# Kernel tuning notes

Hardware: AMD Instinct MI355X
Metric: run time of the kernel (lower is better)

Reference implementation:

```python
import jax, jax.numpy as jnp
import numpy as np

N = 128
INSTANCES = 64
EMBED_DIM = 256
HIDDEN = 1024
BATCH = 2048


def _kaiming(key, dims):
    # matches custom_kaiming: randn * sqrt(2 / dims[-2])
    return jax.random.normal(key, dims, dtype=jnp.float32) * np.sqrt(2.0 / float(dims[-2])).astype(np.float32)


def setup_inputs() -> dict:
    key = jax.random.key(0)
    k_a, k_el, k_er, k_lin, k_un = jax.random.split(key, 5)
    a = jax.random.randint(k_a, (BATCH, 2), 0, N, dtype=jnp.int64 if jax.config.jax_enable_x64 else jnp.int32)
    return {
        "a": a,
        "embedding_left": _kaiming(k_el, (INSTANCES, N, EMBED_DIM)),
        "embedding_right": _kaiming(k_er, (INSTANCES, N, EMBED_DIM)),
        "linear": _kaiming(k_lin, (INSTANCES, EMBED_DIM, HIDDEN)),
        "unembedding": _kaiming(k_un, (INSTANCES, HIDDEN, N)),
    }


def reference(a, embedding_left, embedding_right, linear, unembedding):
    # one-hot @ embedding == direct gather along the vocab axis (same math, O(1) per lookup)
    a1, a2 = a[:, 0], a[:, 1]
    # [instances, batch, embed] -> [batch, instances, embed]
    x1 = jnp.transpose(jnp.take(embedding_left, a1, axis=1), (1, 0, 2))
    x2 = jnp.transpose(jnp.take(embedding_right, a2, axis=1), (1, 0, 2))
    hidden = jnp.einsum('bie,ieh->bih', x1 + x2, linear)
    out = jnp.einsum('bih,ihn->bin', jax.nn.gelu(hidden, approximate=False), unembedding)
    return out
```

## Files before the change

### kernel.cpp

```cpp
#include <hip/hip_runtime.h>
#include <hip/hip_bf16.h>

typedef __bf16 bf16;
typedef __bf16 bf16x4 __attribute__((ext_vector_type(4)));
typedef __bf16 bf16x8 __attribute__((ext_vector_type(8)));
typedef float  f32x4  __attribute__((ext_vector_type(4)));

#define MFMA16(A,B,C) __builtin_amdgcn_mfma_f32_16x16x32_bf16((A),(B),(C),0,0,0)

constexpr int NI    = 64;
constexpr int NN    = 128;
constexpr int E     = 256;
constexpr int HID   = 1024;
constexpr int BATCH = 2048;
constexpr int BM    = 128;
constexpr int BH    = 64;
constexpr int W1P   = E  + 8;
constexpr int W2P   = BH + 8;
constexpr int HP    = BH + 8;

__device__ __forceinline__ float fast_gelu(float x) {
    float p = 1.5957691216f * __builtin_fmaf(0.044715f * x * x, x, x);
    return x * __builtin_amdgcn_rcpf(1.0f + __expf(-p));
}

__global__ __launch_bounds__(256, 2) void mlp3_fused(
    const int*   __restrict__ a,
    const float* __restrict__ embL,
    const float* __restrict__ embR,
    const float* __restrict__ W1,
    const float* __restrict__ W2,
    float* __restrict__ out)
{
    __shared__ __align__(16) bf16 sW1[BH][W1P];
    __shared__ __align__(16) bf16 sW2[NN][W2P];
    __shared__ __align__(16) bf16 sH [BM][HP];

    const int blk   = blockIdx.x;
    const int xcd   = blk & 7;
    const int j     = blk >> 3;
    const int inst  = xcd + 8 * (j >> 4);
    const int btile = j & 15;

    const int tid  = threadIdx.x;
    const int wave = tid >> 6;
    const int lane = tid & 63;
    const int m = lane & 15;
    const int q = lane >> 4;

    bf16x8 aF[2][8];
    #pragma unroll
    for (int rt = 0; rt < 2; ++rt) {
        const int r  = btile * BM + wave * 32 + rt * 16 + m;
        const int i1 = a[2 * r + 0];
        const int i2 = a[2 * r + 1];
        const float* pl = embL + ((size_t)inst * NN + i1) * E;
        const float* pr = embR + ((size_t)inst * NN + i2) * E;
        #pragma unroll
        for (int ks = 0; ks < 8; ++ks) {
            const int e0 = ks * 32 + q * 8;
            f32x4 l0 = *(const f32x4*)(pl + e0);
            f32x4 l1 = *(const f32x4*)(pl + e0 + 4);
            f32x4 r0 = *(const f32x4*)(pr + e0);
            f32x4 r1 = *(const f32x4*)(pr + e0 + 4);
            bf16x8 s;
            #pragma unroll
            for (int k = 0; k < 4; ++k) {
                s[k]     = (bf16)(l0[k] + r0[k]);
                s[k + 4] = (bf16)(l1[k] + r1[k]);
            }
            aF[rt][ks] = s;
        }
    }

    f32x4 O[2][8];
    #pragma unroll
    for (int rt = 0; rt < 2; ++rt)
        #pragma unroll
        for (int ct = 0; ct < 8; ++ct)
            O[rt][ct] = (f32x4){0.f, 0.f, 0.f, 0.f};

    const int w1_h0 = (tid & 15) * 4;
    const int w1_eq = (tid >> 4) * 4;
    const int w2_n0 = (tid & 31) * 4;
    const int w2_hq = (tid >> 5) * 4;

    #pragma unroll 1
    for (int c = 0; c < HID / BH; ++c) {
        __syncthreads();

        {
            const float* base = W1 + ((size_t)inst * E + w1_eq) * HID + c * BH + w1_h0;
            #pragma unroll
            for (int s = 0; s < 4; ++s) {
                f32x4 v[4];
                #pragma unroll
                for (int k = 0; k < 4; ++k)
                    v[k] = *(const f32x4*)(base + ((size_t)s * 64 + k) * HID);
                #pragma unroll
                for (int jj = 0; jj < 4; ++jj) {
                    bf16x4 w;
                    #pragma unroll
                    for (int k = 0; k < 4; ++k) w[k] = (bf16)v[k][jj];
                    *(bf16x4*)&sW1[w1_h0 + jj][s * 64 + w1_eq] = w;
                }
            }
        }
        {
            const float* base = W2 + ((size_t)inst * HID + c * BH + w2_hq) * NN + w2_n0;
            #pragma unroll
            for (int s = 0; s < 2; ++s) {
                f32x4 v[4];
                #pragma unroll
                for (int k = 0; k < 4; ++k)
                    v[k] = *(const f32x4*)(base + ((size_t)s * 32 + k) * NN);
                #pragma unroll
                for (int jj = 0; jj < 4; ++jj) {
                    bf16x4 w;
                    #pragma unroll
                    for (int k = 0; k < 4; ++k) w[k] = (bf16)v[k][jj];
                    *(bf16x4*)&sW2[w2_n0 + jj][s * 32 + w2_hq] = w;
                }
            }
        }
        __syncthreads();

        f32x4 S[2][4];
        #pragma unroll
        for (int rt = 0; rt < 2; ++rt)
            #pragma unroll
            for (int ct = 0; ct < 4; ++ct) S[rt][ct] = (f32x4){0.f, 0.f, 0.f, 0.f};
        #pragma unroll
        for (int ks = 0; ks < 8; ++ks) {
            #pragma unroll
            for (int ct = 0; ct < 4; ++ct) {
                bf16x8 b = *(const bf16x8*)&sW1[ct * 16 + m][ks * 32 + q * 8];
                S[0][ct] = MFMA16(aF[0][ks], b, S[0][ct]);
                S[1][ct] = MFMA16(aF[1][ks], b, S[1][ct]);
            }
        }

        #pragma unroll
        for (int rt = 0; rt < 2; ++rt)
            #pragma unroll
            for (int ct = 0; ct < 4; ++ct)
                #pragma unroll
                for (int rr = 0; rr < 4; ++rr)
                    sH[wave * 32 + rt * 16 + q * 4 + rr][ct * 16 + m] =
                        (bf16)fast_gelu(S[rt][ct][rr]);
        asm volatile("s_waitcnt lgkmcnt(0)" ::: "memory");

        #pragma unroll
        for (int k2 = 0; k2 < 2; ++k2) {
            bf16x8 h0 = *(const bf16x8*)&sH[wave * 32 +  0 + m][k2 * 32 + q * 8];
            bf16x8 h1 = *(const bf16x8*)&sH[wave * 32 + 16 + m][k2 * 32 + q * 8];
            #pragma unroll
            for (int ct = 0; ct < 8; ++ct) {
                bf16x8 b = *(const bf16x8*)&sW2[ct * 16 + m][k2 * 32 + q * 8];
                O[0][ct] = MFMA16(h0, b, O[0][ct]);
                O[1][ct] = MFMA16(h1, b, O[1][ct]);
            }
        }
    }

    #pragma unroll
    for (int rt = 0; rt < 2; ++rt)
        #pragma unroll
        for (int ct = 0; ct < 8; ++ct)
            #pragma unroll
            for (int rr = 0; rr < 4; ++rr) {
                const int b = btile * BM + wave * 32 + rt * 16 + q * 4 + rr;
                const int n = ct * 16 + m;
                out[((size_t)b * NI + inst) * NN + n] = O[rt][ct][rr];
            }
}

extern "C" void kernel_launch(void* const* d_in, const int* in_sizes, int n_in,
                              void* d_out, int out_size, void* d_ws, size_t ws_size,
                              hipStream_t stream)
{
    const int*   a    = (const int*)d_in[0];
    const float* embL = (const float*)d_in[1];
    const float* embR = (const float*)d_in[2];
    const float* lin  = (const float*)d_in[3];
    const float* une  = (const float*)d_in[4];
    float* out = (float*)d_out;

    const int nblocks = (BATCH / BM) * NI;
    mlp3_fused<<<nblocks, 256, 0, stream>>>(a, embL, embR, lin, une, out);
}
```

Baseline: 353.5 us.

## Pre-transpose weights to bf16, DMA double-buffer into LDS, double batch tile

Adds a prep kernel that transposes and converts W1 and W2 to bf16 in workspace with an XOR swizzle. The main kernel then streams these tiles straight into double-buffered LDS with global_load_lds, overlapping the next chunk's load with current compute. The batch tile is doubled to 256 rows so each weight chunk is reused across more rows. The cost is two extra prep launches each call, one block per CU instead of two, and more accumulator registers.

Measured after the change: 381.8 us. 8.0% more time.

```diff
diff --git a/kernel.cpp b/kernel.cpp
--- a/kernel.cpp
+++ b/kernel.cpp
@@ -13,10 +13,9 @@
 constexpr int E     = 256;
 constexpr int HID   = 1024;
 constexpr int BATCH = 2048;
-constexpr int BM    = 128;
+constexpr int BM    = 256;
 constexpr int BH    = 64;
-constexpr int W1P   = E  + 8;
-constexpr int W2P   = BH + 8;
+constexpr int NCH   = HID / BH;
 constexpr int HP    = BH + 8;
 
 __device__ __forceinline__ float fast_gelu(float x) {
@@ -24,23 +23,62 @@
     return x * __builtin_amdgcn_rcpf(1.0f + __expf(-p));
 }
 
-__global__ __launch_bounds__(256, 2) void mlp3_fused(
+__device__ __forceinline__ void load_lds16(const void* gp, void* lp) {
+    __builtin_amdgcn_global_load_lds(
+        (const __attribute__((address_space(1))) unsigned int*)gp,
+        (__attribute__((address_space(3))) unsigned int*)lp, 16, 0, 0);
+}
+
+__global__ __launch_bounds__(256) void prep_t(
+    const float* __restrict__ in, bf16* __restrict__ out, int R, int C)
+{
+    __shared__ float t[64][132];
+    const int inst = blockIdx.z;
+    const int r0 = blockIdx.x * 64;
+    const int c0 = blockIdx.y * 128;
+    const int tid = threadIdx.x;
+
+    const float* ip = in + ((size_t)inst * R + r0) * C + c0;
+    const int tr = tid >> 5, tc4 = tid & 31;
+    #pragma unroll
+    for (int i = 0; i < 8; ++i) {
+        const int r = i * 8 + tr;
+        *(f32x4*)&t[r][tc4 * 4] = *(const f32x4*)(ip + (size_t)r * C + tc4 * 4);
+    }
+    __syncthreads();
+
+    const int c  = c0 + (tid >> 1);
+    const int pg = (tid & 1) * 4;
+    bf16* ob = out + (size_t)(inst * (size_t)C + c) * R + (size_t)(r0 + pg * 8);
+    #pragma unroll
+    for (int k = 0; k < 4; ++k) {
+        const int p = pg + k;
+        const int u = p ^ (c & 7);
+        bf16x8 w;
+        #pragma unroll
+        for (int j = 0; j < 8; ++j) w[j] = (bf16)t[u * 8 + j][tid >> 1];
+        *(bf16x8*)(ob + k * 8) = w;
+    }
+}
+
+template <bool PRET>
+__global__ __launch_bounds__(256, 1) void mlp3_fused(
     const int*   __restrict__ a,
     const float* __restrict__ embL,
     const float* __restrict__ embR,
-    const float* __restrict__ W1,
-    const float* __restrict__ W2,
+    const void*  __restrict__ W1v,
+    const void*  __restrict__ W2v,
     float* __restrict__ out)
 {
-    __shared__ __align__(16) bf16 sW1[BH][W1P];
-    __shared__ __align__(16) bf16 sW2[NN][W2P];
-    __shared__ __align__(16) bf16 sH [BM][HP];
+    __shared__ __align__(16) bf16 sW1[2][BH][E];
+    __shared__ __align__(16) bf16 sW2[2][NN][BH];
+    __shared__ __align__(16) bf16 sH[BM][HP];
 
     const int blk   = blockIdx.x;
     const int xcd   = blk & 7;
     const int j     = blk >> 3;
-    const int inst  = xcd + 8 * (j >> 4);
-    const int btile = j & 15;
+    const int inst  = xcd + 8 * (j >> 3);
+    const int btile = j & 7;
 
     const int tid  = threadIdx.x;
     const int wave = tid >> 6;
@@ -48,14 +86,37 @@
     const int m = lane & 15;
     const int q = lane >> 4;
 
-    bf16x8 aF[2][8];
-    #pragma unroll
-    for (int rt = 0; rt < 2; ++rt) {
-        const int r  = btile * BM + wave * 32 + rt * 16 + m;
-        const int i1 = a[2 * r + 0];
-        const int i2 = a[2 * r + 1];
-        const float* pl = embL + ((size_t)inst * NN + i1) * E;
-        const float* pr = embR + ((size_t)inst * NN + i2) * E;
+    const bf16* W1T = (const bf16*)W1v;
+    const bf16* W2T = (const bf16*)W2v;
+
+    auto issue_dma = [&](int c, int b) {
+        const char* g1 = (const char*)(W1T + ((size_t)inst * HID + c * BH) * E);
+        char* l1 = (char*)&sW1[b][0][0];
+        #pragma unroll
+        for (int i = 0; i < 8; ++i) {
+            const int off = (wave * 8 + i) * 1024;
+            load_lds16(g1 + off + lane * 16, l1 + off);
+        }
+        char* l2 = (char*)&sW2[b][0][0];
+        #pragma unroll
+        for (int i = 0; i < 4; ++i) {
+            const int k = wave * 4 + i;
+            const int n = k * 8 + (lane >> 3);
+            const char* g2 = (const char*)(W2T + ((size_t)inst * NN + n) * HID)
+                             + c * 128 + (lane & 7) * 16;
+            load_lds16(g2, l2 + k * 1024);
+        }
+    };
+
+    if (PRET) issue_dma(0, 0);
+
+    bf16x8 aF[4][8];
+    #pragma unroll
+    for (int rt = 0; rt < 4; ++rt) {
+        const int r = btile * BM + wave * 64 + rt * 16 + m;
+        const int2 av = *(const int2*)(a + 2 * r);
+        const float* pl = embL + ((size_t)inst * 128 + av.x) * E;
+        const float* pr = embR + ((size_t)inst * 128 + av.y) * E;
         #pragma unroll
         for (int ks = 0; ks < 8; ++ks) {
             const int e0 = ks * 32 + q * 8;
@@ -73,103 +134,114 @@
         }
     }
 
-    f32x4 O[2][8];
-    #pragma unroll
-    for (int rt = 0; rt < 2; ++rt)
+    f32x4 O[4][8];
+    #pragma unroll
+    for (int rt = 0; rt < 4; ++rt)
         #pragma unroll
         for (int ct = 0; ct < 8; ++ct)
             O[rt][ct] = (f32x4){0.f, 0.f, 0.f, 0.f};
 
-    const int w1_h0 = (tid & 15) * 4;
-    const int w1_eq = (tid >> 4) * 4;
-    const int w2_n0 = (tid & 31) * 4;
-    const int w2_hq = (tid >> 5) * 4;
-
     #pragma unroll 1
-    for (int c = 0; c < HID / BH; ++c) {
+    for (int c = 0; c < NCH; ++c) {
+        const int buf = c & 1;
+
+        if (!PRET) {
+            __syncthreads();
+            const float* W1f = (const float*)W1v;
+            const float* W2f = (const float*)W2v;
+            {
+                const int h4 = (tid & 15) * 4, e4 = (tid >> 4) * 4;
+                char* base = (char*)&sW1[0][0][0];
+                #pragma unroll
+                for (int s = 0; s < 4; ++s) {
+                    f32x4 v[4];
+                    #pragma unroll
+                    for (int k = 0; k < 4; ++k)
+                        v[k] = *(const f32x4*)(W1f + ((size_t)inst * E + s * 64 + e4 + k) * HID + c * BH + h4);
+                    const int U = s * 8 + (tid >> 5), sub = (tid >> 4) & 1;
+                    #pragma unroll
+                    for (int jj = 0; jj < 4; ++jj) {
+                        const int row = h4 + jj;
+                        bf16x4 w;
+                        #pragma unroll
+                        for (int k = 0; k < 4; ++k) w[k] = (bf16)v[k][jj];
+                        *(bf16x4*)(base + row * 512 + (U ^ (row & 7)) * 16 + sub * 8) = w;
+                    }
+                }
+            }
+            {
+                const int n4 = (tid & 31) * 4, hq = (tid >> 5) * 4;
+                char* base = (char*)&sW2[0][0][0];
+                #pragma unroll
+                for (int s = 0; s < 2; ++s) {
+                    f32x4 v[4];
+                    #pragma unroll
+                    for (int k = 0; k < 4; ++k)
+                        v[k] = *(const f32x4*)(W2f + ((size_t)inst * HID + c * BH + s * 32 + hq + k) * NN + n4);
+                    const int U = s * 4 + (tid >> 6), sub = (tid >> 5) & 1;
+                    #pragma unroll
+                    for (int jj = 0; jj < 4; ++jj) {
+                        const int row = n4 + jj;
+                        bf16x4 w;
+                        #pragma unroll
+                        for (int k = 0; k < 4; ++k) w[k] = (bf16)v[k][jj];
+                        *(bf16x4*)(base + row * 128 + (U ^ (row & 7)) * 16 + sub * 8) = w;
+                    }
+                }
+            }
+        }
+
         __syncthreads();
-
-        {
-            const float* base = W1 + ((size_t)inst * E + w1_eq) * HID + c * BH + w1_h0;
-            #pragma unroll
-            for (int s = 0; s < 4; ++s) {
-                f32x4 v[4];
-                #pragma unroll
-                for (int k = 0; k < 4; ++k)
-                    v[k] = *(const f32x4*)(base + ((size_t)s * 64 + k) * HID);
-                #pragma unroll
-                for (int jj = 0; jj < 4; ++jj) {
-                    bf16x4 w;
-                    #pragma unroll
-                    for (int k = 0; k < 4; ++k) w[k] = (bf16)v[k][jj];
-                    *(bf16x4*)&sW1[w1_h0 + jj][s * 64 + w1_eq] = w;
-                }
-            }
-        }
-        {
-            const float* base = W2 + ((size_t)inst * HID + c * BH + w2_hq) * NN + w2_n0;
-            #pragma unroll
-            for (int s = 0; s < 2; ++s) {
-                f32x4 v[4];
-                #pragma unroll
-                for (int k = 0; k < 4; ++k)
-                    v[k] = *(const f32x4*)(base + ((size_t)s * 32 + k) * NN);
-                #pragma unroll
-                for (int jj = 0; jj < 4; ++jj) {
-                    bf16x4 w;
-                    #pragma unroll
-                    for (int k = 0; k < 4; ++k) w[k] = (bf16)v[k][jj];
-                    *(bf16x4*)&sW2[w2_n0 + jj][s * 32 + w2_hq] = w;
-                }
-            }
-        }
-        __syncthreads();
-
-        f32x4 S[2][4];
-        #pragma unroll
-        for (int rt = 0; rt < 2; ++rt)
-            #pragma unroll
-            for (int ct = 0; ct < 4; ++ct) S[rt][ct] = (f32x4){0.f, 0.f, 0.f, 0.f};
-        #pragma unroll
-        for (int ks = 0; ks < 8; ++ks) {
-            #pragma unroll
-            for (int ct = 0; ct < 4; ++ct) {
-                bf16x8 b = *(const bf16x8*)&sW1[ct * 16 + m][ks * 32 + q * 8];
-                S[0][ct] = MFMA16(aF[0][ks], b, S[0][ct]);
-                S[1][ct] = MFMA16(aF[1][ks], b, S[1][ct]);
-            }
-        }
-
-        #pragma unroll
-        for (int rt = 0; rt < 2; ++rt)
-            #pragma unroll
-            for (int ct = 0; ct < 4; ++ct)
+        if (PRET && c + 1 < NCH) issue_dma(c + 1, buf ^ 1);
+        const int rb = PRET ? buf : 0;
+
+        #pragma unroll
+        for (int ct = 0; ct < 4; ++ct) {
+            f32x4 S[4];
+            #pragma unroll
+            for (int rt = 0; rt < 4; ++rt) S[rt] = (f32x4){0.f, 0.f, 0.f, 0.f};
+            const char* rowp = (const char*)&sW1[rb][ct * 16 + m][0];
+            #pragma unroll
+            for (int ks = 0; ks < 8; ++ks) {
+                const int u = (ks * 4 + q) ^ (m & 7);
+                bf16x8 b = *(const bf16x8*)(rowp + u * 16);
+                #pragma unroll
+                for (int rt = 0; rt < 4; ++rt)
+                    S[rt] = MFMA16(aF[rt][ks], b, S[rt]);
+            }
+            #pragma unroll
+            for (int rt = 0; rt < 4; ++rt)
                 #pragma unroll
                 for (int rr = 0; rr < 4; ++rr)
-                    sH[wave * 32 + rt * 16 + q * 4 + rr][ct * 16 + m] =
-                        (bf16)fast_gelu(S[rt][ct][rr]);
+                    sH[wave * 64 + rt * 16 + q * 4 + rr][ct * 16 + m] =
+                        (bf16)fast_gelu(S[rt][rr]);
+        }
         asm volatile("s_waitcnt lgkmcnt(0)" ::: "memory");
 
         #pragma unroll
         for (int k2 = 0; k2 < 2; ++k2) {
-            bf16x8 h0 = *(const bf16x8*)&sH[wave * 32 +  0 + m][k2 * 32 + q * 8];
-            bf16x8 h1 = *(const bf16x8*)&sH[wave * 32 + 16 + m][k2 * 32 + q * 8];
+            bf16x8 h[4];
+            #pragma unroll
+            for (int rt = 0; rt < 4; ++rt)
+                h[rt] = *(const bf16x8*)&sH[wave * 64 + rt * 16 + m][k2 * 32 + q * 8];
             #pragma unroll
             for (int ct = 0; ct < 8; ++ct) {
-                bf16x8 b = *(const bf16x8*)&sW2[ct * 16 + m][k2 * 32 + q * 8];
-                O[0][ct] = MFMA16(h0, b, O[0][ct]);
-                O[1][ct] = MFMA16(h1, b, O[1][ct]);
-            }
-        }
-    }
-
-    #pragma unroll
-    for (int rt = 0; rt < 2; ++rt)
+                const int u = (k2 * 4 + q) ^ (m & 7);
+                bf16x8 b = *(const bf16x8*)((const char*)&sW2[rb][ct * 16 + m][0] + u * 16);
+                #pragma unroll
+                for (int rt = 0; rt < 4; ++rt)
+                    O[rt][ct] = MFMA16(h[rt], b, O[rt][ct]);
+            }
+        }
+    }
+
+    #pragma unroll
+    for (int rt = 0; rt < 4; ++rt)
         #pragma unroll
         for (int ct = 0; ct < 8; ++ct)
             #pragma unroll
             for (int rr = 0; rr < 4; ++rr) {
-                const int b = btile * BM + wave * 32 + rt * 16 + q * 4 + rr;
+                const int b = btile * BM + wave * 64 + rt * 16 + q * 4 + rr;
                 const int n = ct * 16 + m;
                 out[((size_t)b * NI + inst) * NN + n] = O[rt][ct][rr];
             }
@@ -186,6 +258,21 @@
     const float* une  = (const float*)d_in[4];
     float* out = (float*)d_out;
 
+    const size_t w1t_elems = (size_t)NI * HID * E;
+    const size_t w2t_elems = (size_t)NI * NN * HID;
+    const size_t need = (w1t_elems + w2t_elems) * sizeof(bf16);
+
     const int nblocks = (BATCH / BM) * NI;
-    mlp3_fused<<<nblocks, 256, 0, stream>>>(a, embL, embR, lin, une, out);
-}
+
+    if (ws_size >= need) {
+        bf16* w1t = (bf16*)d_ws;
+        bf16* w2t = w1t + w1t_elems;
+        prep_t<<<dim3(E / 64, HID / 128, NI), 256, 0, stream>>>(lin, w1t, E, HID);
+        prep_t<<<dim3(HID / 64, NN / 128, NI), 256, 0, stream>>>(une, w2t, HID, NN);
+        mlp3_fused<true><<<nblocks, 256, 0, stream>>>(
+            a, embL, embR, (const void*)w1t, (const void*)w2t, out);
+    } else {
+        mlp3_fused<false><<<nblocks, 256, 0, stream>>>(
+            a, embL, embR, (const void*)lin, (const void*)une, out);
+    }
+}
```
